# Kernel tuning notes

Hardware: AMD Instinct MI355X
Metric: run time of the kernel (lower is better)

The kernel has to match this reference:

```python
import jax, jax.numpy as jnp
import numpy as np
from jax import lax

CH, GROUP = 32, 8  # channel=32, subchannel=4 -> group=8

def conv2d(x, w, b, pad):
    # x: [B,C,H,W], w: [O,I,kh,kw]
    out = lax.conv_general_dilated(x, w, (1, 1), [(pad, pad), (pad, pad)],
                                   dimension_numbers=("NCHW", "OIHW", "NCHW"))
    return out + b[None, :, None, None]

def pconv(x, w, b):
    # 1x1 conv as einsum; w: [O,I]
    return jnp.einsum("oi,bihw->bohw", w, x) + b[None, :, None, None]

def setup_inputs() -> dict:
    key = jax.random.key(0)
    ks = jax.random.split(key, 32)
    s = 0.05
    d = {
        "x": jax.random.normal(ks[0], (8, CH, 64, 64), jnp.float32),
        "y": jax.random.normal(ks[1], (8, 1, 64, 64), jnp.float32),
        "conv_w": jax.random.normal(ks[2], (CH, CH + GROUP, 3, 3), jnp.float32) * s,
        "conv_b": jax.random.normal(ks[3], (CH,), jnp.float32) * s,
        "score_w": jax.random.normal(ks[4], (1, CH, 3, 3), jnp.float32) * s,
        "score_b": jax.random.normal(ks[5], (1,), jnp.float32) * s,
        "c132_w": jax.random.normal(ks[6], (32, 1, 3, 3), jnp.float32) * s,
        "c132_b": jax.random.normal(ks[7], (32,), jnp.float32) * s,
        "q1_w": jax.random.normal(ks[8], (32, 32), jnp.float32) * s,
        "q1_b": jax.random.normal(ks[9], (32,), jnp.float32) * s,
        "k1_w": jax.random.normal(ks[10], (32, 32), jnp.float32) * s,
        "k1_b": jax.random.normal(ks[11], (32,), jnp.float32) * s,
        "q2_w": jax.random.normal(ks[12], (32, 32), jnp.float32) * s,
        "q2_b": jax.random.normal(ks[13], (32,), jnp.float32) * s,
        "k2_w": jax.random.normal(ks[14], (32, 32), jnp.float32) * s,
        "k2_b": jax.random.normal(ks[15], (32,), jnp.float32) * s,
        "q3_w": jax.random.normal(ks[16], (32, 32), jnp.float32) * s,
        "q3_b": jax.random.normal(ks[17], (32,), jnp.float32) * s,
        "k3_w": jax.random.normal(ks[18], (32, 32), jnp.float32) * s,
        "k3_b": jax.random.normal(ks[19], (32,), jnp.float32) * s,
        "conv6_w": jax.random.normal(ks[20], (32, 64), jnp.float32) * s,
        "conv6_b": jax.random.normal(ks[21], (32,), jnp.float32) * s,
    }
    return d

def reference(x, y, conv_w, conv_b, score_w, score_b, c132_w, c132_b,
              q1_w, q1_b, k1_w, k1_b, q2_w, q2_b, k2_w, k2_b,
              q3_w, q3_b, k3_w, k3_b, conv6_w, conv6_b):
    B, C, H, W = x.shape
    sub = C // GROUP
    # group-wise chunk + interleave y: [x_g0, y, x_g1, y, ...]
    xg = x.reshape(B, GROUP, sub, H, W)
    yb = jnp.broadcast_to(y[:, None], (B, GROUP, 1, H, W))
    x_cat = jnp.concatenate([xg, yb], axis=2).reshape(B, C + GROUP, H, W)
    x1_co = jax.nn.relu(conv2d(x_cat, conv_w, conv_b, 1))        # [B,32,H,W]
    x2_co = conv2d(y, c132_w, c132_b, 1)                          # [B,32,H,W]

    HW = H * W
    x_query1 = pconv(x1_co, q1_w, q1_b).reshape(B, 32, HW)
    x_key1 = pconv(x1_co, k1_w, k1_b).reshape(B, 32, HW)
    x_query2 = pconv(x1_co, q2_w, q2_b).reshape(B, 32, HW)
    x_key2 = pconv(x1_co, k2_w, k2_b).reshape(B, 32, HW)
    y_query = pconv(x2_co, q3_w, q3_b).reshape(B, 32, HW)
    y_key = pconv(x2_co, k3_w, k3_b).reshape(B, 32, HW)

    # spatial attention [B, HW, HW]
    x_hw = jax.nn.softmax(jnp.einsum("bcn,bcm->bnm", x_query1, x_key2), axis=-1)
    # channel attention [B, 32, 32]
    x_c = jax.nn.softmax(jnp.einsum("bcn,bdn->bcd", x_key1, x_query2), axis=-1)

    xy_hw = jnp.einsum("bcn,bnm->bcm", y_query, x_hw).reshape(B, 32, H, W)
    xy_c = jnp.einsum("bcd,bcn->bdn", x_c, y_key).reshape(B, 32, H, W)

    out_final = pconv(jnp.concatenate([xy_hw, xy_c], axis=1), conv6_w, conv6_b)
    x_out = x + out_final
    y_out = y + conv2d(x_out, score_w, score_b, 1)
    return (x_out, y_out)
```

## Files before the change

kernel.cpp:

```cpp
#include <hip/hip_runtime.h>
#include <hip/hip_bf16.h>
#include <math.h>

#define HW 4096

typedef short bf16x8_t __attribute__((ext_vector_type(8)));
typedef float f32x16_t __attribute__((ext_vector_type(16)));
typedef unsigned int u32;
typedef unsigned int u32x4_t __attribute__((ext_vector_type(4)));
typedef int i32x2_t __attribute__((ext_vector_type(2)));

union castu { u32x4_t u; bf16x8_t s; };

static __device__ __forceinline__ unsigned short f2bf(float f){
    union { __bf16 b; unsigned short u; } c; c.b = (__bf16)f; return c.u;
}
static __device__ __forceinline__ u32 pk2(float lo, float hi){
    return ((u32)f2bf(hi) << 16) | (u32)f2bf(lo);
}
static __device__ __forceinline__ bf16x8_t ldb(const unsigned short* p){
    return *reinterpret_cast<const bf16x8_t*>(p);
}
static __device__ __forceinline__ bf16x8_t ld_xs(const unsigned short* p){
    uint2 lo = *(const uint2*)(p);
    uint2 hi = *(const uint2*)(p + 4);
    castu c; c.u = (u32x4_t){lo.x, lo.y, hi.x, hi.y};
    return c.s;
}
static __device__ __forceinline__ f32x16_t mfma32(bf16x8_t a, bf16x8_t b, f32x16_t c){
    return __builtin_amdgcn_mfma_f32_32x32x16_bf16(a, b, c, 0, 0, 0);
}
static __device__ __forceinline__ float ex2(float x){
    return __builtin_amdgcn_exp2f(x);
}
static __device__ __forceinline__ void cd2bfrag(const u32 P[8], bf16x8_t& b0, bf16x8_t& b1){
    i32x2_t s02 = __builtin_amdgcn_permlane32_swap((int)P[0], (int)P[2], false, false);
    i32x2_t s13 = __builtin_amdgcn_permlane32_swap((int)P[1], (int)P[3], false, false);
    i32x2_t s46 = __builtin_amdgcn_permlane32_swap((int)P[4], (int)P[6], false, false);
    i32x2_t s57 = __builtin_amdgcn_permlane32_swap((int)P[5], (int)P[7], false, false);
    castu c0, c1;
    c0.u = (u32x4_t){ (u32)s02[0], (u32)s13[0], (u32)s02[1], (u32)s13[1] };
    c1.u = (u32x4_t){ (u32)s46[0], (u32)s57[0], (u32)s46[1], (u32)s57[1] };
    b0 = c0.s; b1 = c1.s;
}

#define LOG2E 1.44269504088896340736f

__global__ __launch_bounds__(256, 1) void k_front_mfma(
    const float* __restrict__ x, const float* __restrict__ y,
    const float* __restrict__ conv_w, const float* __restrict__ conv_b,
    const float* __restrict__ c132_w, const float* __restrict__ c132_b,
    const float* __restrict__ q1w, const float* __restrict__ q1b,
    const float* __restrict__ k1w, const float* __restrict__ k1b,
    const float* __restrict__ q2w, const float* __restrict__ q2b,
    const float* __restrict__ k2w, const float* __restrict__ k2b,
    const float* __restrict__ q3w, const float* __restrict__ q3b,
    const float* __restrict__ k3w, const float* __restrict__ k3b,
    float* __restrict__ K1, float* __restrict__ Q2, float* __restrict__ YQ,
    unsigned short* __restrict__ Q1t, unsigned short* __restrict__ K2t,
    unsigned short* __restrict__ YKt)
{
    __shared__ unsigned short xs[4 * 68 * 36];
    __shared__ float ys[4 * 68];
    __shared__ u32 wplane[18 * 4 * 64];
    __shared__ u32 wyplane[4 * 64];
    __shared__ u32 c1plane[4 * 64];

    int tid = threadIdx.x;
    int h0 = blockIdx.x * 2, b = blockIdx.y;

    #pragma unroll
    for (int i = 0; i < 32; ++i){
        int idx = i * 256 + tid;
        int w = idx & 63, ic = (idx >> 6) & 31, dr = idx >> 11;
        int hr = h0 - 1 + dr;
        float v = (hr >= 0 && hr < 64) ? x[((b * 32 + ic) << 12) + (hr << 6) + w] : 0.f;
        xs[(dr * 68 + w + 1) * 36 + ic] = f2bf(v);
    }
    {
        int dr = tid >> 6, ic = tid & 31, side = (tid >> 5) & 1;
        xs[(dr * 68 + (side ? 65 : 0)) * 36 + ic] = 0;
    }
    for (int idx = tid; idx < 272; idx += 256){
        int dr = idx / 68, wp = idx % 68;
        int hr = h0 - 1 + dr, w = wp - 1;
        ys[idx] = (hr >= 0 && hr < 64 && w >= 0 && w < 64) ? y[(b << 12) + (hr << 6) + w] : 0.f;
    }
    for (int e = tid; e < 4608; e += 256){
        int f = e >> 8, wi = (e >> 6) & 3, ln = e & 63;
        int t = f >> 1, j = f & 1, hh = ln >> 5, ll = ln & 31;
        int ic0 = 16 * j + 8 * hh + 2 * wi;
        int co0 = 5 * (ic0 >> 2) + (ic0 & 3);
        int ic1 = ic0 + 1;
        int co1 = 5 * (ic1 >> 2) + (ic1 & 3);
        wplane[e] = pk2(conv_w[ll * 360 + co0 * 9 + t], conv_w[ll * 360 + co1 * 9 + t]);
    }
    {
        int wi = tid >> 6, ln = tid & 63, hh = ln >> 5, ll = ln & 31;
        u32 vy = 0, vc = 0;
        if (hh == 0){
            int t0 = 2 * wi, t1 = 2 * wi + 1;
            float s0 = 0.f, s1 = 0.f;
            #pragma unroll
            for (int g = 0; g < 8; ++g){
                s0 += conv_w[ll * 360 + (5 * g + 4) * 9 + t0];
                s1 += conv_w[ll * 360 + (5 * g + 4) * 9 + t1];
            }
            vy = pk2(s0, s1);
            vc = pk2(c132_w[ll * 9 + t0], c132_w[ll * 9 + t1]);
        } else if (wi == 0){
            float s0 = 0.f;
            #pragma unroll
            for (int g = 0; g < 8; ++g) s0 += conv_w[ll * 360 + (5 * g + 4) * 9 + 8];
            vy = pk2(s0, 0.f);
            vc = pk2(c132_w[ll * 9 + 8], 0.f);
        }
        wyplane[wi * 64 + ln] = vy;
        c1plane[wi * 64 + ln] = vc;
    }
    __syncthreads();

    int lane = tid & 63, wid = tid >> 6;
    int l31 = lane & 31, h = lane >> 5;
    int wr = wid >> 1, toff = (wid & 1) * 32;
    int wpB = toff + l31;

    bf16x8_t wA[18];
    #pragma unroll
    for (int f = 0; f < 18; ++f){
        castu c;
        c.u = (u32x4_t){ wplane[(f * 4 + 0) * 64 + lane], wplane[(f * 4 + 1) * 64 + lane],
                         wplane[(f * 4 + 2) * 64 + lane], wplane[(f * 4 + 3) * 64 + lane] };
        wA[f] = c.s;
    }
    castu wyf, c1f;
    wyf.u = (u32x4_t){ wyplane[lane], wyplane[64 + lane], wyplane[128 + lane], wyplane[192 + lane] };
    c1f.u = (u32x4_t){ c1plane[lane], c1plane[64 + lane], c1plane[128 + lane], c1plane[192 + lane] };

    float yv[8];
    #pragma unroll
    for (int i = 0; i < 8; ++i){
        int tt = 8 * h + i;
        yv[i] = (tt < 9) ? ys[(wr + tt / 3) * 68 + wpB + (tt % 3)] : 0.f;
    }
    castu yf;
    yf.u = (u32x4_t){ pk2(yv[0], yv[1]), pk2(yv[2], yv[3]), pk2(yv[4], yv[5]), pk2(yv[6], yv[7]) };

    f32x16_t accE, accO, accY, acc2;
    #pragma unroll
    for (int r = 0; r < 16; ++r){
        int oc = (r & 3) + 8 * (r >> 2) + 4 * h;
        accE[r] = 0.f; accO[r] = 0.f;
        accY[r] = conv_b[oc]; acc2[r] = c132_b[oc];
    }
    #pragma unroll
    for (int t = 0; t < 9; ++t){
        int base = ((wr + t / 3) * 68 + wpB + (t % 3)) * 36 + 8 * h;
        bf16x8_t b0 = ld_xs(xs + base);
        bf16x8_t b1 = ld_xs(xs + base + 16);
        if (t & 1){
            accO = mfma32(wA[t * 2 + 0], b0, accO);
            accO = mfma32(wA[t * 2 + 1], b1, accO);
        } else {
            accE = mfma32(wA[t * 2 + 0], b0, accE);
            accE = mfma32(wA[t * 2 + 1], b1, accE);
        }
    }
    accY = mfma32(wyf.s, yf.s, accY);
    acc2 = mfma32(c1f.s, yf.s, acc2);

    f32x16_t x1v;
    #pragma unroll
    for (int r = 0; r < 16; ++r){
        float v = accE[r] + accO[r] + accY[r];
        x1v[r] = v > 0.f ? v : 0.f;
    }
    u32 P[8];
    bf16x8_t x1b0, x1b1, x2b0, x2b1;
    #pragma unroll
    for (int t2 = 0; t2 < 8; ++t2) P[t2] = pk2(x1v[2 * t2], x1v[2 * t2 + 1]);
    cd2bfrag(P, x1b0, x1b1);
    #pragma unroll
    for (int t2 = 0; t2 < 8; ++t2) P[t2] = pk2(acc2[2 * t2], acc2[2 * t2 + 1]);
    cd2bfrag(P, x2b0, x2b1);

    int pxg = (h0 + wr) * 64 + toff + l31;
    size_t bf_base = ((size_t)b * HW + pxg) * 32;

    {
        f32x16_t a;
        #pragma unroll
        for (int r = 0; r < 16; ++r) a[r] = q1b[(r & 3) + 8 * (r >> 2) + 4 * h];
        const float* p0 = q1w + l31 * 32 + 8 * h;
        castu w0, w1;
        w0.u = (u32x4_t){ pk2(p0[0],p0[1]), pk2(p0[2],p0[3]), pk2(p0[4],p0[5]), pk2(p0[6],p0[7]) };
        w1.u = (u32x4_t){ pk2(p0[16],p0[17]), pk2(p0[18],p0[19]), pk2(p0[20],p0[21]), pk2(p0[22],p0[23]) };
        a = mfma32(w0.s, x1b0, a);
        a = mfma32(w1.s, x1b1, a);
        u32 Q[8];
        #pragma unroll
        for (int t2 = 0; t2 < 8; ++t2) Q[t2] = pk2(a[2 * t2] * LOG2E, a[2 * t2 + 1] * LOG2E);
        *(uint2*)(Q1t + bf_base + 4 * h)      = make_uint2(Q[0], Q[1]);
        *(uint2*)(Q1t + bf_base + 8 + 4 * h)  = make_uint2(Q[2], Q[3]);
        *(uint2*)(Q1t + bf_base + 16 + 4 * h) = make_uint2(Q[4], Q[5]);
        *(uint2*)(Q1t + bf_base + 24 + 4 * h) = make_uint2(Q[6], Q[7]);
    }
    {
        f32x16_t a;
        #pragma unroll
        for (int r = 0; r < 16; ++r) a[r] = k1b[(r & 3) + 8 * (r >> 2) + 4 * h];
        const float* p0 = k1w + l31 * 32 + 8 * h;
        castu w0, w1;
        w0.u = (u32x4_t){ pk2(p0[0],p0[1]), pk2(p0[2],p0[3]), pk2(p0[4],p0[5]), pk2(p0[6],p0[7]) };
        w1.u = (u32x4_t){ pk2(p0[16],p0[17]), pk2(p0[18],p0[19]), pk2(p0[20],p0[21]), pk2(p0[22],p0[23]) };
        a = mfma32(w0.s, x1b0, a);
        a = mfma32(w1.s, x1b1, a);
        #pragma unroll
        for (int r = 0; r < 16; ++r)
            K1[(b * 32 + (r & 3) + 8 * (r >> 2) + 4 * h) * HW + pxg] = a[r];
    }
    {
        f32x16_t a;
        #pragma unroll
        for (int r = 0; r < 16; ++r) a[r] = q2b[(r & 3) + 8 * (r >> 2) + 4 * h];
        const float* p0 = q2w + l31 * 32 + 8 * h;
        castu w0, w1;
        w0.u = (u32x4_t){ pk2(p0[0],p0[1]), pk2(p0[2],p0[3]), pk2(p0[4],p0[5]), pk2(p0[6],p0[7]) };
        w1.u = (u32x4_t){ pk2(p0[16],p0[17]), pk2(p0[18],p0[19]), pk2(p0[20],p0[21]), pk2(p0[22],p0[23]) };
        a = mfma32(w0.s, x1b0, a);
        a = mfma32(w1.s, x1b1, a);
        #pragma unroll
        for (int r = 0; r < 16; ++r)
            Q2[(b * 32 + (r & 3) + 8 * (r >> 2) + 4 * h) * HW + pxg] = a[r];
    }
    {
        f32x16_t a;
        #pragma unroll
        for (int r = 0; r < 16; ++r) a[r] = k2b[(r & 3) + 8 * (r >> 2) + 4 * h];
        const float* p0 = k2w + l31 * 32 + 8 * h;
        castu w0, w1;
        w0.u = (u32x4_t){ pk2(p0[0],p0[1]), pk2(p0[2],p0[3]), pk2(p0[4],p0[5]), pk2(p0[6],p0[7]) };
        w1.u = (u32x4_t){ pk2(p0[16],p0[17]), pk2(p0[18],p0[19]), pk2(p0[20],p0[21]), pk2(p0[22],p0[23]) };
        a = mfma32(w0.s, x1b0, a);
        a = mfma32(w1.s, x1b1, a);
        u32 Q[8];
        #pragma unroll
        for (int t2 = 0; t2 < 8; ++t2) Q[t2] = pk2(a[2 * t2], a[2 * t2 + 1]);
        *(uint2*)(K2t + bf_base + 4 * h)      = make_uint2(Q[0], Q[1]);
        *(uint2*)(K2t + bf_base + 8 + 4 * h)  = make_uint2(Q[2], Q[3]);
        *(uint2*)(K2t + bf_base + 16 + 4 * h) = make_uint2(Q[4], Q[5]);
        *(uint2*)(K2t + bf_base + 24 + 4 * h) = make_uint2(Q[6], Q[7]);
    }
    {
        f32x16_t a;
        #pragma unroll
        for (int r = 0; r < 16; ++r) a[r] = q3b[(r & 3) + 8 * (r >> 2) + 4 * h];
        const float* p0 = q3w + l31 * 32 + 8 * h;
        castu w0, w1;
        w0.u = (u32x4_t){ pk2(p0[0],p0[1]), pk2(p0[2],p0[3]), pk2(p0[4],p0[5]), pk2(p0[6],p0[7]) };
        w1.u = (u32x4_t){ pk2(p0[16],p0[17]), pk2(p0[18],p0[19]), pk2(p0[20],p0[21]), pk2(p0[22],p0[23]) };
        a = mfma32(w0.s, x2b0, a);
        a = mfma32(w1.s, x2b1, a);
        #pragma unroll
        for (int r = 0; r < 16; ++r)
            YQ[(b * 32 + (r & 3) + 8 * (r >> 2) + 4 * h) * HW + pxg] = a[r];
    }
    {
        f32x16_t a;
        #pragma unroll
        for (int r = 0; r < 16; ++r) a[r] = k3b[(r & 3) + 8 * (r >> 2) + 4 * h];
        const float* p0 = k3w + l31 * 32 + 8 * h;
        castu w0, w1;
        w0.u = (u32x4_t){ pk2(p0[0],p0[1]), pk2(p0[2],p0[3]), pk2(p0[4],p0[5]), pk2(p0[6],p0[7]) };
        w1.u = (u32x4_t){ pk2(p0[16],p0[17]), pk2(p0[18],p0[19]), pk2(p0[20],p0[21]), pk2(p0[22],p0[23]) };
        a = mfma32(w0.s, x2b0, a);
        a = mfma32(w1.s, x2b1, a);
        u32 Q[8];
        #pragma unroll
        for (int t2 = 0; t2 < 8; ++t2) Q[t2] = pk2(a[2 * t2], a[2 * t2 + 1]);
        *(uint2*)(YKt + bf_base + 4 * h)      = make_uint2(Q[0], Q[1]);
        *(uint2*)(YKt + bf_base + 8 + 4 * h)  = make_uint2(Q[2], Q[3]);
        *(uint2*)(YKt + bf_base + 16 + 4 * h) = make_uint2(Q[4], Q[5]);
        *(uint2*)(YKt + bf_base + 24 + 4 * h) = make_uint2(Q[6], Q[7]);
    }
}

__global__ __launch_bounds__(256) void k_chan_part(
    const float* __restrict__ K1, const float* __restrict__ Q2,
    float* __restrict__ Scp)
{
    __shared__ float k1s[128 * 33];
    __shared__ float q2s[128 * 33];
    int b = blockIdx.x & 7;
    int chunk = blockIdx.x >> 3;
    int n0 = chunk * 128;
    int t = threadIdx.x;
    for (int i = 0; i < 16; ++i){
        int idx = i * 256 + t;
        int c = idx >> 7, nl = idx & 127;
        k1s[nl * 33 + c] = K1[(b * 32 + c) * HW + n0 + nl];
        q2s[nl * 33 + c] = Q2[(b * 32 + c) * HW + n0 + nl];
    }
    __syncthreads();
    float acc[4] = {0.f, 0.f, 0.f, 0.f};
    int d = t & 31, c0 = t >> 5;
    for (int nl = 0; nl < 128; ++nl){
        float qv = q2s[nl * 33 + d];
        #pragma unroll
        for (int i = 0; i < 4; ++i)
            acc[i] = fmaf(k1s[nl * 33 + c0 + 8 * i], qv, acc[i]);
    }
    #pragma unroll
    for (int i = 0; i < 4; ++i)
        Scp[(b * 32 + chunk) * 1024 + (c0 + 8 * i) * 32 + d] = acc[i];
}

__global__ __launch_bounds__(1024) void k_chan_fin(
    const float* __restrict__ Scp, const float* __restrict__ c6w,
    float* __restrict__ M2)
{
    __shared__ float pc[32 * 33];
    int b = blockIdx.x;
    int t = threadIdx.x;
    int c = t >> 5, d = t & 31;
    float s = 0.f;
    for (int k = 0; k < 32; ++k) s += Scp[(b * 32 + k) * 1024 + t];
    float mx = s;
    #pragma unroll
    for (int off = 16; off >= 1; off >>= 1) mx = fmaxf(mx, __shfl_xor(mx, off));
    float e = __expf(s - mx);
    float sum = e;
    #pragma unroll
    for (int off = 16; off >= 1; off >>= 1) sum += __shfl_xor(sum, off);
    pc[c * 33 + d] = e / sum;
    __syncthreads();
    int o = t >> 5, cc = t & 31;
    float m2 = 0.f;
    #pragma unroll
    for (int dd = 0; dd < 32; ++dd)
        m2 = fmaf(c6w[o * 64 + 32 + dd], pc[cc * 33 + dd], m2);
    M2[b * 1024 + o * 32 + cc] = m2;
}

__global__ __launch_bounds__(256, 4) void k_stats_mfma(
    const unsigned short* __restrict__ Q1t, const unsigned short* __restrict__ K2t,
    const float* __restrict__ YQ, unsigned short* __restrict__ YQ2)
{
    __shared__ float red[4][16][64];
    __shared__ float ls[32];
    int t = threadIdx.x, wid = t >> 6, lane = t & 63;
    int l31 = lane & 31, h = lane >> 5;
    int b = blockIdx.x & 7, ntile = blockIdx.x >> 3;
    int n0 = ntile * 32;
    const unsigned short* q = Q1t + (size_t)b * 131072;
    const unsigned short* k = K2t + (size_t)b * 131072;
    bf16x8_t a0 = ldb(q + (size_t)(n0 + l31) * 32 + 8 * h);
    bf16x8_t a1 = ldb(q + (size_t)(n0 + l31) * 32 + 16 + 8 * h);
    float accl[16];
    #pragma unroll
    for (int r = 0; r < 16; ++r) accl[r] = 0.f;

    const unsigned short* kp = k + ((size_t)(wid << 10) + l31) * 32 + 8 * h;
    bf16x8_t b0 = ldb(kp), b1 = ldb(kp + 16);
    f32x16_t s_cur;
    #pragma unroll
    for (int r = 0; r < 16; ++r) s_cur[r] = 0.f;
    s_cur = mfma32(a0, b0, s_cur);
    s_cur = mfma32(a1, b1, s_cur);
    kp += 1024;
    bf16x8_t b0n = ldb(kp), b1n = ldb(kp + 16);

    #pragma unroll 4
    for (int i = 0; i < 32; ++i){
        f32x16_t s_nxt;
        #pragma unroll
        for (int r = 0; r < 16; ++r) s_nxt[r] = 0.f;
        __builtin_amdgcn_s_setprio(1);
        s_nxt = mfma32(a0, b0n, s_nxt);
        s_nxt = mfma32(a1, b1n, s_nxt);
        __builtin_amdgcn_s_setprio(0);
        kp += (i < 30) ? 1024 : 0;
        bf16x8_t b0nn = ldb(kp), b1nn = ldb(kp + 16);
        #pragma unroll
        for (int r = 0; r < 16; ++r) accl[r] += ex2(s_cur[r]);
        s_cur = s_nxt; b0n = b0nn; b1n = b1nn;
    }
    #pragma unroll
    for (int r = 0; r < 16; ++r) red[wid][r][lane] = accl[r];
    __syncthreads();
    if (wid == 0){
        #pragma unroll
        for (int r = 0; r < 16; ++r){
            float v = red[0][r][lane] + red[1][r][lane] + red[2][r][lane] + red[3][r][lane];
            #pragma unroll
            for (int off = 16; off >= 1; off >>= 1) v += __shfl_xor(v, off);
            if (l31 == 0)
                ls[(r & 3) + 8 * (r >> 2) + 4 * h] = 1.0f / v;
        }
    }
    __syncthreads();
    size_t obase = ((size_t)(b * 128 + ntile)) * 1024;
    #pragma unroll
    for (int p = 0; p < 4; ++p){
        int idx = (p << 8) + t;
        int c = idx >> 5, n = idx & 31;
        size_t g = (size_t)(b * 32 + c) * HW + n0 + n;
        YQ2[obase + idx] = f2bf(YQ[g] * ls[n]);
    }
}

__global__ __launch_bounds__(256, 4) void k_attn_mfma(
    const unsigned short* __restrict__ Q1t, const unsigned short* __restrict__ K2t,
    const unsigned short* __restrict__ YKt, const unsigned short* __restrict__ YQ2,
    const float* __restrict__ M2, const float* __restrict__ c6w, const float* __restrict__ c6b,
    const float* __restrict__ x, float* __restrict__ xout)
{
    __shared__ float red[4][16][64];
    int t = threadIdx.x, wid = t >> 6, lane = t & 63;
    int l31 = lane & 31, h = lane >> 5;
    int b = blockIdx.x & 7, mtile = blockIdx.x >> 3;
    int m0 = mtile * 32;
    size_t boff = (size_t)b * 131072;
    const unsigned short* qb = Q1t + boff;
    const unsigned short* kb = K2t + boff;

    bf16x8_t kb0 = ldb(kb + (size_t)(m0 + l31) * 32 + 8 * h);
    bf16x8_t kb1 = ldb(kb + (size_t)(m0 + l31) * 32 + 16 + 8 * h);

    f32x16_t oacc;
    #pragma unroll
    for (int r = 0; r < 16; ++r) oacc[r] = 0.f;

    const unsigned short* qp = qb + ((size_t)(wid << 10) + l31) * 32 + 8 * h;
    const unsigned short* yp = YQ2 + ((size_t)(b * 128 + (wid << 5)) * 32 + l31) * 32 + 8 * h;

    bf16x8_t a0 = ldb(qp), a1 = ldb(qp + 16);
    bf16x8_t y0 = ldb(yp), y1 = ldb(yp + 16);
    f32x16_t s_cur;
    #pragma unroll
    for (int r = 0; r < 16; ++r) s_cur[r] = 0.f;
    s_cur = mfma32(a0, kb0, s_cur);
    s_cur = mfma32(a1, kb1, s_cur);
    qp += 1024; yp += 1024;
    bf16x8_t a0n = ldb(qp), a1n = ldb(qp + 16);
    bf16x8_t y0n = ldb(yp), y1n = ldb(yp + 16);

    #pragma unroll 4
    for (int i = 0; i < 32; ++i){
        f32x16_t s_nxt;
        #pragma unroll
        for (int r = 0; r < 16; ++r) s_nxt[r] = 0.f;
        __builtin_amdgcn_s_setprio(1);
        s_nxt = mfma32(a0n, kb0, s_nxt);
        s_nxt = mfma32(a1n, kb1, s_nxt);
        __builtin_amdgcn_s_setprio(0);
        int adv = (i < 30) ? 1024 : 0;
        qp += adv; yp += adv;
        bf16x8_t a0nn = ldb(qp), a1nn = ldb(qp + 16);
        bf16x8_t y0nn = ldb(yp), y1nn = ldb(yp + 16);
        u32 P[8];
        #pragma unroll
        for (int tt = 0; tt < 8; ++tt)
            P[tt] = pk2(ex2(s_cur[2 * tt]), ex2(s_cur[2 * tt + 1]));
        bf16x8_t e0, e1;
        cd2bfrag(P, e0, e1);
        __builtin_amdgcn_s_setprio(1);
        oacc = mfma32(y0, e0, oacc);
        oacc = mfma32(y1, e1, oacc);
        __builtin_amdgcn_s_setprio(0);
        s_cur = s_nxt;
        a0n = a0nn; a1n = a1nn;
        y0 = y0n; y1 = y1n; y0n = y0nn; y1n = y1nn;
    }
    #pragma unroll
    for (int r = 0; r < 16; ++r) red[wid][r][lane] = oacc[r];
    __syncthreads();
    if (wid != 0) return;
    #pragma unroll
    for (int r = 0; r < 16; ++r)
        oacc[r] = red[0][r][lane] + red[1][r][lane] + red[2][r][lane] + red[3][r][lane];

    u32 P[8];
    #pragma unroll
    for (int tt = 0; tt < 8; ++tt) P[tt] = pk2(oacc[2 * tt], oacc[2 * tt + 1]);
    bf16x8_t xb0, xb1;
    cd2bfrag(P, xb0, xb1);

    const float* w1p = c6w + l31 * 64;
    const float* m2p = M2 + b * 1024 + l31 * 32;
    int cb0 = 8 * h, cb1 = 16 + 8 * h;
    castu wa0, wa1, ma0, ma1;
    wa0.u = (u32x4_t){ pk2(w1p[cb0], w1p[cb0+1]), pk2(w1p[cb0+2], w1p[cb0+3]),
                       pk2(w1p[cb0+4], w1p[cb0+5]), pk2(w1p[cb0+6], w1p[cb0+7]) };
    wa1.u = (u32x4_t){ pk2(w1p[cb1], w1p[cb1+1]), pk2(w1p[cb1+2], w1p[cb1+3]),
                       pk2(w1p[cb1+4], w1p[cb1+5]), pk2(w1p[cb1+6], w1p[cb1+7]) };
    ma0.u = (u32x4_t){ pk2(m2p[cb0], m2p[cb0+1]), pk2(m2p[cb0+2], m2p[cb0+3]),
                       pk2(m2p[cb0+4], m2p[cb0+5]), pk2(m2p[cb0+6], m2p[cb0+7]) };
    ma1.u = (u32x4_t){ pk2(m2p[cb1], m2p[cb1+1]), pk2(m2p[cb1+2], m2p[cb1+3]),
                       pk2(m2p[cb1+4], m2p[cb1+5]), pk2(m2p[cb1+6], m2p[cb1+7]) };
    const unsigned short* ykp = YKt + boff + (size_t)(m0 + l31) * 32;
    bf16x8_t ykb0 = ldb(ykp + 8 * h);
    bf16x8_t ykb1 = ldb(ykp + 16 + 8 * h);

    f32x16_t facc;
    #pragma unroll
    for (int r = 0; r < 16; ++r) facc[r] = c6b[(r & 3) + 8 * (r >> 2) + 4 * h];
    facc = mfma32(wa0.s, xb0, facc);
    facc = mfma32(wa1.s, xb1, facc);
    facc = mfma32(ma0.s, ykb0, facc);
    facc = mfma32(ma1.s, ykb1, facc);

    #pragma unroll
    for (int r = 0; r < 16; ++r){
        int o = (r & 3) + 8 * (r >> 2) + 4 * h;
        size_t gi = ((size_t)(b * 32 + o) << 12) + m0 + l31;
        xout[gi] = x[gi] + facc[r];
    }
}

__global__ __launch_bounds__(256) void k_score(
    const float* __restrict__ xout, const float* __restrict__ y,
    const float* __restrict__ sw, const float* __restrict__ sb,
    float* __restrict__ yout)
{
    __shared__ float xs[3][32][66];
    __shared__ float red[4][64];
    int tid = threadIdx.x;
    int b = blockIdx.x & 7, h = blockIdx.x >> 3;
    for (int i = 0; i < 24; ++i){
        int idx = i * 256 + tid;
        int w = idx & 63, ic = (idx >> 6) & 31, dr = idx >> 11;
        int hr = h + dr - 1;
        xs[dr][ic][1 + w] = (hr >= 0 && hr < 64) ? xout[((b * 32 + ic) << 12) + (hr << 6) + w] : 0.f;
    }
    if (tid < 96){ xs[tid >> 5][tid & 31][0] = 0.f; }
    else if (tid < 192){ int u = tid - 96; xs[u >> 5][u & 31][65] = 0.f; }
    __syncthreads();
    int w = tid & 63, icg = tid >> 6;
    float p = 0.f;
    #pragma unroll
    for (int i = 0; i < 8; ++i){
        int ic = icg * 8 + i;
        #pragma unroll
        for (int tap = 0; tap < 9; ++tap)
            p = fmaf(sw[ic * 9 + tap], xs[tap / 3][ic][w + tap % 3], p);
    }
    red[icg][w] = p;
    __syncthreads();
    if (tid < 64){
        int px = (h << 6) + tid;
        yout[b * HW + px] = y[b * HW + px] + sb[0]
                          + red[0][tid] + red[1][tid] + red[2][tid] + red[3][tid];
    }
}

extern "C" void kernel_launch(void* const* d_in, const int* in_sizes, int n_in,
                              void* d_out, int out_size, void* d_ws, size_t ws_size,
                              hipStream_t stream)
{
    (void)in_sizes; (void)n_in; (void)out_size; (void)ws_size;
    const float* x      = (const float*)d_in[0];
    const float* y      = (const float*)d_in[1];
    const float* conv_w = (const float*)d_in[2];
    const float* conv_b = (const float*)d_in[3];
    const float* score_w= (const float*)d_in[4];
    const float* score_b= (const float*)d_in[5];
    const float* c132_w = (const float*)d_in[6];
    const float* c132_b = (const float*)d_in[7];
    const float* q1w = (const float*)d_in[8];  const float* q1b = (const float*)d_in[9];
    const float* k1w = (const float*)d_in[10]; const float* k1b = (const float*)d_in[11];
    const float* q2w = (const float*)d_in[12]; const float* q2b = (const float*)d_in[13];
    const float* k2w = (const float*)d_in[14]; const float* k2b = (const float*)d_in[15];
    const float* q3w = (const float*)d_in[16]; const float* q3b = (const float*)d_in[17];
    const float* k3w = (const float*)d_in[18]; const float* k3b = (const float*)d_in[19];
    const float* c6w = (const float*)d_in[20]; const float* c6b = (const float*)d_in[21];

    float* ws = (float*)d_ws;
    const size_t SZ = 1048576;
    float* Scp = ws;
    float* M2  = ws + 262144;
    float* K1  = ws + 2 * SZ;
    float* Q2  = ws + 3 * SZ;
    float* YQf = ws + 4 * SZ;
    unsigned short* Q1t = (unsigned short*)(ws + 5 * SZ);
    unsigned short* K2t = (unsigned short*)(ws + 5 * SZ + SZ / 2);
    unsigned short* YKt = (unsigned short*)(ws + 6 * SZ);
    unsigned short* YQ2 = (unsigned short*)(ws + 6 * SZ + SZ / 2);

    float* xout = (float*)d_out;
    float* yout = xout + SZ;

    k_front_mfma<<<dim3(32, 8), 256, 0, stream>>>(
        x, y, conv_w, conv_b, c132_w, c132_b,
        q1w, q1b, k1w, k1b, q2w, q2b, k2w, k2b, q3w, q3b, k3w, k3b,
        K1, Q2, YQf, Q1t, K2t, YKt);
    k_chan_part<<<256, 256, 0, stream>>>(K1, Q2, Scp);
    k_chan_fin<<<8, 1024, 0, stream>>>(Scp, c6w, M2);
    k_stats_mfma<<<1024, 256, 0, stream>>>(Q1t, K2t, YQf, YQ2);
    k_attn_mfma<<<1024, 256, 0, stream>>>(Q1t, K2t, YKt, YQ2, M2, c6w, c6b, x, xout);
    k_score<<<512, 256, 0, stream>>>(xout, y, score_w, score_b, yout);
}
```

Baseline: 107.1 us.

## Replace hardware exp2 with bit-trick exp2 and double waves per attention block

Swaps the v_exp_f32-based exp2 in the stats and attention kernels for a Schraudolph-style FMA-plus-int-convert approximation. In the attention kernel it packs the bf16 high halves with a byte-permute. Both kernels go from 4 to 8 waves per block, and each wave handles half as many key tiles, with the cross-wave reduction widened to match. The aim is to cut transcendental-unit pressure and raise latency hiding. The trade-off is a noticeably less accurate exponential (piecewise linear mantissa) and more LDS for the reduction.

Measured after the change: 280.6 us. 162% more time.

```diff
diff --git a/kernel.cpp b/kernel.cpp
--- a/kernel.cpp
+++ b/kernel.cpp
@@ -30,9 +30,23 @@
 static __device__ __forceinline__ f32x16_t mfma32(bf16x8_t a, bf16x8_t b, f32x16_t c){
     return __builtin_amdgcn_mfma_f32_32x32x16_bf16(a, b, c, 0, 0, 0);
 }
-static __device__ __forceinline__ float ex2(float x){
-    return __builtin_amdgcn_exp2f(x);
-}
+
+#define EXP2_MAG  8388608.0f
+#define EXP2_BIAS 1064986816.0f
+
+static __device__ __forceinline__ float fexp2(float x){
+    return __int_as_float((int)fmaf(x, EXP2_MAG, EXP2_BIAS));
+}
+static __device__ __forceinline__ u32 pkexp2(float lo, float hi){
+    u32 i0 = (u32)(int)fmaf(lo, EXP2_MAG, EXP2_BIAS);
+    u32 i1 = (u32)(int)fmaf(hi, EXP2_MAG, EXP2_BIAS);
+#if __has_builtin(__builtin_amdgcn_perm)
+    return __builtin_amdgcn_perm(i1, i0, 0x07060302u);
+#else
+    return (i1 & 0xFFFF0000u) | (i0 >> 16);
+#endif
+}
+
 static __device__ __forceinline__ void cd2bfrag(const u32 P[8], bf16x8_t& b0, bf16x8_t& b1){
     i32x2_t s02 = __builtin_amdgcn_permlane32_swap((int)P[0], (int)P[2], false, false);
     i32x2_t s13 = __builtin_amdgcn_permlane32_swap((int)P[1], (int)P[3], false, false);
@@ -342,11 +356,11 @@
     M2[b * 1024 + o * 32 + cc] = m2;
 }
 
-__global__ __launch_bounds__(256, 4) void k_stats_mfma(
+__global__ __launch_bounds__(512, 8) void k_stats_mfma(
     const unsigned short* __restrict__ Q1t, const unsigned short* __restrict__ K2t,
     const float* __restrict__ YQ, unsigned short* __restrict__ YQ2)
 {
-    __shared__ float red[4][16][64];
+    __shared__ float red[8][16][64];
     __shared__ float ls[32];
     int t = threadIdx.x, wid = t >> 6, lane = t & 63;
     int l31 = lane & 31, h = lane >> 5;
@@ -360,7 +374,7 @@
     #pragma unroll
     for (int r = 0; r < 16; ++r) accl[r] = 0.f;
 
-    const unsigned short* kp = k + ((size_t)(wid << 10) + l31) * 32 + 8 * h;
+    const unsigned short* kp = k + ((size_t)(wid << 9) + l31) * 32 + 8 * h;
     bf16x8_t b0 = ldb(kp), b1 = ldb(kp + 16);
     f32x16_t s_cur;
     #pragma unroll
@@ -371,7 +385,7 @@
     bf16x8_t b0n = ldb(kp), b1n = ldb(kp + 16);
 
     #pragma unroll 4
-    for (int i = 0; i < 32; ++i){
+    for (int i = 0; i < 16; ++i){
         f32x16_t s_nxt;
         #pragma unroll
         for (int r = 0; r < 16; ++r) s_nxt[r] = 0.f;
@@ -379,10 +393,10 @@
         s_nxt = mfma32(a0, b0n, s_nxt);
         s_nxt = mfma32(a1, b1n, s_nxt);
         __builtin_amdgcn_s_setprio(0);
-        kp += (i < 30) ? 1024 : 0;
+        kp += (i < 14) ? 1024 : 0;
         bf16x8_t b0nn = ldb(kp), b1nn = ldb(kp + 16);
         #pragma unroll
-        for (int r = 0; r < 16; ++r) accl[r] += ex2(s_cur[r]);
+        for (int r = 0; r < 16; ++r) accl[r] += fexp2(s_cur[r]);
         s_cur = s_nxt; b0n = b0nn; b1n = b1nn;
     }
     #pragma unroll
@@ -391,7 +405,9 @@
     if (wid == 0){
         #pragma unroll
         for (int r = 0; r < 16; ++r){
-            float v = red[0][r][lane] + red[1][r][lane] + red[2][r][lane] + red[3][r][lane];
+            float v = 0.f;
+            #pragma unroll
+            for (int w = 0; w < 8; ++w) v += red[w][r][lane];
             #pragma unroll
             for (int off = 16; off >= 1; off >>= 1) v += __shfl_xor(v, off);
             if (l31 == 0)
@@ -401,21 +417,21 @@
     __syncthreads();
     size_t obase = ((size_t)(b * 128 + ntile)) * 1024;
     #pragma unroll
-    for (int p = 0; p < 4; ++p){
-        int idx = (p << 8) + t;
+    for (int p = 0; p < 2; ++p){
+        int idx = (p << 9) + t;
         int c = idx >> 5, n = idx & 31;
         size_t g = (size_t)(b * 32 + c) * HW + n0 + n;
         YQ2[obase + idx] = f2bf(YQ[g] * ls[n]);
     }
 }
 
-__global__ __launch_bounds__(256, 4) void k_attn_mfma(
+__global__ __launch_bounds__(512, 8) void k_attn_mfma(
     const unsigned short* __restrict__ Q1t, const unsigned short* __restrict__ K2t,
     const unsigned short* __restrict__ YKt, const unsigned short* __restrict__ YQ2,
     const float* __restrict__ M2, const float* __restrict__ c6w, const float* __restrict__ c6b,
     const float* __restrict__ x, float* __restrict__ xout)
 {
-    __shared__ float red[4][16][64];
+    __shared__ float red[8][16][64];
     int t = threadIdx.x, wid = t >> 6, lane = t & 63;
     int l31 = lane & 31, h = lane >> 5;
     int b = blockIdx.x & 7, mtile = blockIdx.x >> 3;
@@ -431,8 +447,8 @@
     #pragma unroll
     for (int r = 0; r < 16; ++r) oacc[r] = 0.f;
 
-    const unsigned short* qp = qb + ((size_t)(wid << 10) + l31) * 32 + 8 * h;
-    const unsigned short* yp = YQ2 + ((size_t)(b * 128 + (wid << 5)) * 32 + l31) * 32 + 8 * h;
+    const unsigned short* qp = qb + ((size_t)(wid << 9) + l31) * 32 + 8 * h;
+    const unsigned short* yp = YQ2 + ((size_t)(b * 128 + (wid << 4)) * 32 + l31) * 32 + 8 * h;
 
     bf16x8_t a0 = ldb(qp), a1 = ldb(qp + 16);
     bf16x8_t y0 = ldb(yp), y1 = ldb(yp + 16);
@@ -446,7 +462,7 @@
     bf16x8_t y0n = ldb(yp), y1n = ldb(yp + 16);
 
     #pragma unroll 4
-    for (int i = 0; i < 32; ++i){
+    for (int i = 0; i < 16; ++i){
         f32x16_t s_nxt;
         #pragma unroll
         for (int r = 0; r < 16; ++r) s_nxt[r] = 0.f;
@@ -454,14 +470,14 @@
         s_nxt = mfma32(a0n, kb0, s_nxt);
         s_nxt = mfma32(a1n, kb1, s_nxt);
         __builtin_amdgcn_s_setprio(0);
-        int adv = (i < 30) ? 1024 : 0;
+        int adv = (i < 14) ? 1024 : 0;
         qp += adv; yp += adv;
         bf16x8_t a0nn = ldb(qp), a1nn = ldb(qp + 16);
         bf16x8_t y0nn = ldb(yp), y1nn = ldb(yp + 16);
         u32 P[8];
         #pragma unroll
         for (int tt = 0; tt < 8; ++tt)
-            P[tt] = pk2(ex2(s_cur[2 * tt]), ex2(s_cur[2 * tt + 1]));
+            P[tt] = pkexp2(s_cur[2 * tt], s_cur[2 * tt + 1]);
         bf16x8_t e0, e1;
         cd2bfrag(P, e0, e1);
         __builtin_amdgcn_s_setprio(1);
@@ -477,8 +493,12 @@
     __syncthreads();
     if (wid != 0) return;
     #pragma unroll
-    for (int r = 0; r < 16; ++r)
-        oacc[r] = red[0][r][lane] + red[1][r][lane] + red[2][r][lane] + red[3][r][lane];
+    for (int r = 0; r < 16; ++r){
+        float v = 0.f;
+        #pragma unroll
+        for (int w = 0; w < 8; ++w) v += red[w][r][lane];
+        oacc[r] = v;
+    }
 
     u32 P[8];
     #pragma unroll
@@ -596,7 +616,7 @@
         K1, Q2, YQf, Q1t, K2t, YKt);
     k_chan_part<<<256, 256, 0, stream>>>(K1, Q2, Scp);
     k_chan_fin<<<8, 1024, 0, stream>>>(Scp, c6w, M2);
-    k_stats_mfma<<<1024, 256, 0, stream>>>(Q1t, K2t, YQf, YQ2);
-    k_attn_mfma<<<1024, 256, 0, stream>>>(Q1t, K2t, YKt, YQ2, M2, c6w, c6b, x, xout);
+    k_stats_mfma<<<1024, 512, 0, stream>>>(Q1t, K2t, YQf, YQ2);
+    k_attn_mfma<<<1024, 512, 0, stream>>>(Q1t, K2t, YKt, YQ2, M2, c6w, c6b, x, xout);
     k_score<<<512, 256, 0, stream>>>(xout, y, score_w, score_b, yout);
 }
```
